# Kernel optimization log

Measured on AMD Instinct MI355X. Metric: run time of the kernel, lower is better.

Reference implementation:

```python
import jax, jax.numpy as jnp
import numpy as np

B, T, C, HS = 256, 256, 384, 64

def setup_inputs() -> dict:
    key = jax.random.key(0)
    ks = jax.random.split(key, 7)
    return {
        "x": jax.random.normal(ks[0], (B, T, C), dtype=jnp.float32),
        "Wq": jax.random.normal(ks[1], (C, HS), dtype=jnp.float32) * (C ** -0.5),
        "bq": jax.random.normal(ks[2], (HS,), dtype=jnp.float32) * 0.02,
        "Wk": jax.random.normal(ks[3], (C, HS), dtype=jnp.float32) * (C ** -0.5),
        "bk": jax.random.normal(ks[4], (HS,), dtype=jnp.float32) * 0.02,
        "Wv": jax.random.normal(ks[5], (C, HS), dtype=jnp.float32) * (C ** -0.5),
        "bv": jax.random.normal(ks[6], (HS,), dtype=jnp.float32) * 0.02,
    }

def reference(x, Wq, bq, Wk, bk, Wv, bv):
    # single-head causal self-attention (eval mode: dropout is identity)
    T_ = x.shape[1]
    q = x @ Wq + bq          # [B, T, HS]
    k = x @ Wk + bk          # [B, T, HS]
    v = x @ Wv + bv          # [B, T, HS]
    scale = k.shape[-1] ** -0.5
    att = jnp.einsum("btd,bsd->bts", q, k) * scale   # [B, T, T]
    causal = jnp.tril(jnp.ones((T_, T_), dtype=bool))  # tril buffer
    att = jnp.where(causal, att, -jnp.inf)             # mask future positions
    att = jax.nn.softmax(att, axis=-1)
    return jnp.einsum("bts,bsd->btd", att, v)          # [B, T, HS]
```

## Files before the change

kernel.cpp:

```cpp
#include <hip/hip_runtime.h>
#include <hip/hip_bf16.h>

#define BB 256
#define TT 256
#define CC 384
#define HSS 64

typedef __bf16 bf16_t;
typedef bf16_t bf16x8 __attribute__((ext_vector_type(8)));
typedef bf16_t bf16x4 __attribute__((ext_vector_type(4)));
typedef float f32x4 __attribute__((ext_vector_type(4)));

__device__ __forceinline__ f32x4 mfma16(bf16x8 a, bf16x8 b, f32x4 c) {
    return __builtin_amdgcn_mfma_f32_16x16x32_bf16(a, b, c, 0, 0, 0);
}

__device__ __forceinline__ bf16x8 cvt8(float4 a, float4 b) {
    bf16x8 r;
    r[0] = (bf16_t)a.x; r[1] = (bf16_t)a.y; r[2] = (bf16_t)a.z; r[3] = (bf16_t)a.w;
    r[4] = (bf16_t)b.x; r[5] = (bf16_t)b.y; r[6] = (bf16_t)b.z; r[7] = (bf16_t)b.w;
    return r;
}

typedef __attribute__((address_space(3))) unsigned int lds_uint_t;
typedef const __attribute__((address_space(1))) unsigned int glb_uint_t;
__device__ __forceinline__ void async_cp16(const void* g, void* lds_uniform) {
    __builtin_amdgcn_global_load_lds((glb_uint_t*)g, (lds_uint_t*)lds_uniform, 16, 0, 0);
}

__global__ void prep_w(const float* __restrict__ Wq, const float* __restrict__ Wk,
                       const float* __restrict__ Wv, bf16_t* __restrict__ WtG) {
    int idx = blockIdx.x * 256 + threadIdx.x;
    if (idx >= 192 * 384) return;
    int n = idx / 384, k = idx % 384;
    const float* W = (n < 64) ? Wq : (n < 128) ? Wk : Wv;
    float val = W[k * 64 + (n & 63)];
    int kc = k >> 6, kin = k & 63;
    int c = kin >> 3, e = k & 7;
    int pc = c ^ (n & 7);
    WtG[kc * 12288 + n * 64 + pc * 8 + e] = (bf16_t)val;
}

__global__ __attribute__((amdgpu_flat_work_group_size(512, 512),
                          amdgpu_waves_per_eu(2, 2)))
void head_fused(
    const float* __restrict__ x, const bf16_t* __restrict__ WtG,
    const float* __restrict__ bq, const float* __restrict__ bk, const float* __restrict__ bv,
    float* __restrict__ out) {

    __shared__ bf16_t Wl[2][12288];
    __shared__ uint4 Ksw[2048];
    __shared__ uint4 Vsw[2048];
    __shared__ __align__(16) bf16_t Pb[8 * 640];

    int b = blockIdx.x, tid = threadIdx.x;
    int w = tid >> 6, l = tid & 63, lr = l & 15, lq = l >> 4;
    int Mt[2] = {w, 15 - w};

    float bqv[4], bkv[4], bvv[4];
#pragma unroll
    for (int nt = 0; nt < 4; nt++) {
        bqv[nt] = bq[nt * 16 + lr];
        bkv[nt] = bk[nt * 16 + lr];
        bvv[nt] = bv[nt * 16 + lr];
    }

    const float* xr[2];
    xr[0] = x + ((size_t)b * TT + Mt[0] * 16 + lr) * CC;
    xr[1] = x + ((size_t)b * TT + Mt[1] * 16 + lr) * CC;

    f32x4 acc[2][12];
#pragma unroll
    for (int m = 0; m < 2; m++)
#pragma unroll
        for (int i = 0; i < 12; i++) acc[m][i] = (f32x4){0.f, 0.f, 0.f, 0.f};

    float4 xf[2][2][2];

#define DMA_CHUNK(kc, buf)                                                   \
    {                                                                        \
        const bf16_t* _src = WtG + (kc) * 12288;                             \
        _Pragma("unroll")                                                    \
        for (int j = 0; j < 3; j++) {                                        \
            int cbase = (j * 8 + w) * 64;   \
            async_cp16(_src + (size_t)(cbase + l) * 8,                       \
                       &Wl[buf][(size_t)cbase * 8]);                         \
        }                                                                    \
    }
#define LOAD_X(kc)                                                           \
    {                                                                        \
        _Pragma("unroll")                                                    \
        for (int m = 0; m < 2; m++)                                          \
            _Pragma("unroll")                                                \
            for (int t = 0; t < 2; t++) {                                    \
                const float* xp = xr[m] + (kc) * 64 + t * 32 + lq * 8;       \
                xf[m][t][0] = *(const float4*)xp;                            \
                xf[m][t][1] = *(const float4*)(xp + 4);                      \
            }                                                                \
    }

    DMA_CHUNK(0, 0);
    LOAD_X(0);

#pragma unroll
    for (int kc = 0; kc < 6; kc++) {
        __syncthreads();
        bf16x8 af[2][2];
#pragma unroll
        for (int m = 0; m < 2; m++)
#pragma unroll
            for (int t = 0; t < 2; t++) af[m][t] = cvt8(xf[m][t][0], xf[m][t][1]);
        if (kc < 5) {
            DMA_CHUNK(kc + 1, (kc + 1) & 1);
            LOAD_X(kc + 1);
        }
        const bf16_t* buf = Wl[kc & 1];
#pragma unroll
        for (int nt = 0; nt < 12; nt++) {
            const bf16_t* wl = buf + (size_t)(nt * 16 + lr) * 64;
#pragma unroll
            for (int t = 0; t < 2; t++) {
                int pc = (t * 4 + lq) ^ (lr & 7);
                bf16x8 bfrag = *(const bf16x8*)(wl + pc * 8);
                acc[0][nt] = mfma16(af[0][t], bfrag, acc[0][nt]);
                acc[1][nt] = mfma16(af[1][t], bfrag, acc[1][nt]);
            }
        }
    }
#undef DMA_CHUNK
#undef LOAD_X

    bf16_t* KswB = (bf16_t*)Ksw;
    bf16_t* VswB = (bf16_t*)Vsw;
#pragma unroll
    for (int m = 0; m < 2; m++) {
#pragma unroll
        for (int nt = 4; nt < 8; nt++) {
            int d = (nt - 4) * 16 + lr;
#pragma unroll
            for (int r = 0; r < 4; r++) {
                int s = Mt[m] * 16 + lq * 4 + r;
                KswB[s * 64 + ((d >> 3) ^ (s & 7)) * 8 + (d & 7)] =
                    (bf16_t)(acc[m][nt][r] + bkv[nt - 4]);
            }
        }
#pragma unroll
        for (int nt = 8; nt < 12; nt++) {
            int d = (nt - 8) * 16 + lr;
            int t0 = Mt[m] * 16 + lq * 4;
            int c = t0 >> 3;
            bf16x4 pk;
#pragma unroll
            for (int r = 0; r < 4; r++) pk[r] = (bf16_t)(acc[m][nt][r] + bvv[nt - 8]);
            *(bf16x4*)(VswB + d * 256 + ((c & ~7) | ((c ^ d) & 7)) * 8 + (t0 & 7)) = pk;
        }
    }
    __syncthreads();

    const float scale2 = 0.125f * 1.4426950408889634f;
    bf16_t* Pw = Pb + w * 640;

#pragma unroll
    for (int m = 0; m < 2; m++) {
        int R0 = Mt[m] * 16;
        int tg = R0 + lr;
        int ktm = Mt[m] >> 1;

        bf16x8 qf[2];
#pragma unroll
        for (int hh = 0; hh < 2; hh++) {
#pragma unroll
            for (int u = 0; u < 2; u++) {
                int nt = 2 * hh + u;
#pragma unroll
                for (int r = 0; r < 4; r++)
                    Pw[(lq * 4 + r) * 40 + u * 16 + lr] =
                        (bf16_t)(acc[m][nt][r] + bqv[nt]);
            }
            qf[hh] = *(const bf16x8*)(Pw + lr * 40 + lq * 8);
        }

        f32x4 oacc[4] = {};
        float sum = 0.f;
#pragma unroll
        for (int kt = 0; kt < 8; kt++) {
            if (kt <= ktm) {
#pragma unroll
                for (int u = 0; u < 2; u++) {
                    int nt = kt * 2 + u;
                    int s = nt * 16 + lr;
                    const uint4* krow = Ksw + s * 8;
                    bf16x8 k0 = __builtin_bit_cast(bf16x8, krow[lq ^ (s & 7)]);
                    bf16x8 k1 = __builtin_bit_cast(bf16x8, krow[(4 + lq) ^ (s & 7)]);
                    f32x4 a = {0.f, 0.f, 0.f, 0.f};
                    a = mfma16(k0, qf[0], a);
                    a = mfma16(k1, qf[1], a);
                    bf16x4 pk;
#pragma unroll
                    for (int r = 0; r < 4; r++) {
                        int sg = nt * 16 + lq * 4 + r;
                        float p = (sg <= tg) ? exp2f(a[r] * scale2) : 0.f;
                        sum += p;
                        pk[r] = (bf16_t)p;
                    }
                    *(bf16x4*)(Pw + lr * 40 + u * 16 + lq * 4) = pk;
                }
                bf16x8 pf = *(const bf16x8*)(Pw + lr * 40 + lq * 8);
#pragma unroll
                for (int dt = 0; dt < 4; dt++) {
                    int d = dt * 16 + lr;
                    int cc = kt * 4 + lq;
                    bf16x8 vf = __builtin_bit_cast(bf16x8,
                        Vsw[d * 32 + ((cc & ~7) | ((cc ^ d) & 7))]);
                    oacc[dt] = mfma16(vf, pf, oacc[dt]);
                }
            }
        }

        sum += __shfl_xor(sum, 16);
        sum += __shfl_xor(sum, 32);
        float inv = 1.0f / sum;

        float* orow = out + ((size_t)b * TT + R0 + lr) * HSS;
#pragma unroll
        for (int dt = 0; dt < 4; dt++) {
            float4 o;
            o.x = oacc[dt][0] * inv;
            o.y = oacc[dt][1] * inv;
            o.z = oacc[dt][2] * inv;
            o.w = oacc[dt][3] * inv;
            *(float4*)(orow + dt * 16 + lq * 4) = o;
        }
    }
}

extern "C" void kernel_launch(void* const* d_in, const int* in_sizes, int n_in,
                              void* d_out, int out_size, void* d_ws, size_t ws_size,
                              hipStream_t stream) {
    const float* x  = (const float*)d_in[0];
    const float* Wq = (const float*)d_in[1];
    const float* bq = (const float*)d_in[2];
    const float* Wk = (const float*)d_in[3];
    const float* bk = (const float*)d_in[4];
    const float* Wv = (const float*)d_in[5];
    const float* bv = (const float*)d_in[6];
    float* out = (float*)d_out;

    bf16_t* WtG = (bf16_t*)d_ws;

    prep_w<<<288, 256, 0, stream>>>(Wq, Wk, Wv, WtG);
    head_fused<<<BB, 512, 0, stream>>>(x, WtG, bq, bk, bv, out);
}
```

Measured before the change: 176.0 us.

## Use 16 waves per block with one query tile per wave

The block grows from 512 to 1024 threads, and each of 16 waves now owns a single 16-row tile instead of a paired front/back tile. Each wave does half the projection MFMAs and needs fewer accumulator registers, which is meant to raise waves per EU and hide latency. The cost is losing the causal load balancing the tile pairing gave: waves with late tiles do up to eight times the attention work of early ones, so the block finishes at the pace of the slowest wave. The weight DMA is split across 16 waves with a conditional second copy.

```diff
diff --git a/kernel.cpp b/kernel.cpp
--- a/kernel.cpp
+++ b/kernel.cpp
@@ -41,8 +41,8 @@
     WtG[kc * 12288 + n * 64 + pc * 8 + e] = (bf16_t)val;
 }
 
-__global__ __attribute__((amdgpu_flat_work_group_size(512, 512),
-                          amdgpu_waves_per_eu(2, 2)))
+__global__ __attribute__((amdgpu_flat_work_group_size(1024, 1024),
+                          amdgpu_waves_per_eu(4, 4)))
 void head_fused(
     const float* __restrict__ x, const bf16_t* __restrict__ WtG,
     const float* __restrict__ bq, const float* __restrict__ bk, const float* __restrict__ bv,
@@ -51,11 +51,11 @@
     __shared__ bf16_t Wl[2][12288];
     __shared__ uint4 Ksw[2048];
     __shared__ uint4 Vsw[2048];
-    __shared__ __align__(16) bf16_t Pb[8 * 640];
+    __shared__ __align__(16) bf16_t Pb[16 * 640];
 
     int b = blockIdx.x, tid = threadIdx.x;
     int w = tid >> 6, l = tid & 63, lr = l & 15, lq = l >> 4;
-    int Mt[2] = {w, 15 - w};
+    int Mt = w;
 
     float bqv[4], bkv[4], bvv[4];
 #pragma unroll
@@ -65,38 +65,34 @@
         bvv[nt] = bv[nt * 16 + lr];
     }
 
-    const float* xr[2];
-    xr[0] = x + ((size_t)b * TT + Mt[0] * 16 + lr) * CC;
-    xr[1] = x + ((size_t)b * TT + Mt[1] * 16 + lr) * CC;
-
-    f32x4 acc[2][12];
-#pragma unroll
-    for (int m = 0; m < 2; m++)
-#pragma unroll
-        for (int i = 0; i < 12; i++) acc[m][i] = (f32x4){0.f, 0.f, 0.f, 0.f};
-
-    float4 xf[2][2][2];
+    const float* xr = x + ((size_t)b * TT + Mt * 16 + lr) * CC;
+
+    f32x4 acc[12];
+#pragma unroll
+    for (int i = 0; i < 12; i++) acc[i] = (f32x4){0.f, 0.f, 0.f, 0.f};
+
+    float4 xf[2][2];
 
 #define DMA_CHUNK(kc, buf)                                                   \
     {                                                                        \
         const bf16_t* _src = WtG + (kc) * 12288;                             \
-        _Pragma("unroll")                                                    \
-        for (int j = 0; j < 3; j++) {                                        \
-            int cbase = (j * 8 + w) * 64;   \
-            async_cp16(_src + (size_t)(cbase + l) * 8,                       \
-                       &Wl[buf][(size_t)cbase * 8]);                         \
+        int cb0 = w * 64;                                                    \
+        async_cp16(_src + (size_t)(cb0 + l) * 8,                             \
+                   &Wl[buf][(size_t)cb0 * 8]);                               \
+        if (w < 8) {                                                         \
+            int cb1 = (16 + w) * 64;                                         \
+            async_cp16(_src + (size_t)(cb1 + l) * 8,                         \
+                       &Wl[buf][(size_t)cb1 * 8]);                           \
         }                                                                    \
     }
 #define LOAD_X(kc)                                                           \
     {                                                                        \
         _Pragma("unroll")                                                    \
-        for (int m = 0; m < 2; m++)                                          \
-            _Pragma("unroll")                                                \
-            for (int t = 0; t < 2; t++) {                                    \
-                const float* xp = xr[m] + (kc) * 64 + t * 32 + lq * 8;       \
-                xf[m][t][0] = *(const float4*)xp;                            \
-                xf[m][t][1] = *(const float4*)(xp + 4);                      \
-            }                                                                \
+        for (int t = 0; t < 2; t++) {                                        \
+            const float* xp = xr + (kc) * 64 + t * 32 + lq * 8;              \
+            xf[t][0] = *(const float4*)xp;                                   \
+            xf[t][1] = *(const float4*)(xp + 4);                             \
+        }                                                                    \
     }
 
     DMA_CHUNK(0, 0);
@@ -105,11 +101,9 @@
 #pragma unroll
     for (int kc = 0; kc < 6; kc++) {
         __syncthreads();
-        bf16x8 af[2][2];
-#pragma unroll
-        for (int m = 0; m < 2; m++)
-#pragma unroll
-            for (int t = 0; t < 2; t++) af[m][t] = cvt8(xf[m][t][0], xf[m][t][1]);
+        bf16x8 af[2];
+#pragma unroll
+        for (int t = 0; t < 2; t++) af[t] = cvt8(xf[t][0], xf[t][1]);
         if (kc < 5) {
             DMA_CHUNK(kc + 1, (kc + 1) & 1);
             LOAD_X(kc + 1);
@@ -122,8 +116,7 @@
             for (int t = 0; t < 2; t++) {
                 int pc = (t * 4 + lq) ^ (lr & 7);
                 bf16x8 bfrag = *(const bf16x8*)(wl + pc * 8);
-                acc[0][nt] = mfma16(af[0][t], bfrag, acc[0][nt]);
-                acc[1][nt] = mfma16(af[1][t], bfrag, acc[1][nt]);
+                acc[nt] = mfma16(af[t], bfrag, acc[nt]);
             }
         }
     }
@@ -133,104 +126,98 @@
     bf16_t* KswB = (bf16_t*)Ksw;
     bf16_t* VswB = (bf16_t*)Vsw;
 #pragma unroll
-    for (int m = 0; m < 2; m++) {
-#pragma unroll
-        for (int nt = 4; nt < 8; nt++) {
-            int d = (nt - 4) * 16 + lr;
-#pragma unroll
-            for (int r = 0; r < 4; r++) {
-                int s = Mt[m] * 16 + lq * 4 + r;
-                KswB[s * 64 + ((d >> 3) ^ (s & 7)) * 8 + (d & 7)] =
-                    (bf16_t)(acc[m][nt][r] + bkv[nt - 4]);
-            }
-        }
-#pragma unroll
-        for (int nt = 8; nt < 12; nt++) {
-            int d = (nt - 8) * 16 + lr;
-            int t0 = Mt[m] * 16 + lq * 4;
-            int c = t0 >> 3;
-            bf16x4 pk;
-#pragma unroll
-            for (int r = 0; r < 4; r++) pk[r] = (bf16_t)(acc[m][nt][r] + bvv[nt - 8]);
-            *(bf16x4*)(VswB + d * 256 + ((c & ~7) | ((c ^ d) & 7)) * 8 + (t0 & 7)) = pk;
-        }
+    for (int nt = 4; nt < 8; nt++) {
+        int d = (nt - 4) * 16 + lr;
+#pragma unroll
+        for (int r = 0; r < 4; r++) {
+            int s = Mt * 16 + lq * 4 + r;
+            KswB[s * 64 + ((d >> 3) ^ (s & 7)) * 8 + (d & 7)] =
+                (bf16_t)(acc[nt][r] + bkv[nt - 4]);
+        }
+    }
+#pragma unroll
+    for (int nt = 8; nt < 12; nt++) {
+        int d = (nt - 8) * 16 + lr;
+        int t0 = Mt * 16 + lq * 4;
+        int c = t0 >> 3;
+        bf16x4 pk;
+#pragma unroll
+        for (int r = 0; r < 4; r++) pk[r] = (bf16_t)(acc[nt][r] + bvv[nt - 8]);
+        *(bf16x4*)(VswB + d * 256 + ((c & ~7) | ((c ^ d) & 7)) * 8 + (t0 & 7)) = pk;
     }
     __syncthreads();
 
     const float scale2 = 0.125f * 1.4426950408889634f;
     bf16_t* Pw = Pb + w * 640;
 
-#pragma unroll
-    for (int m = 0; m < 2; m++) {
-        int R0 = Mt[m] * 16;
-        int tg = R0 + lr;
-        int ktm = Mt[m] >> 1;
-
-        bf16x8 qf[2];
-#pragma unroll
-        for (int hh = 0; hh < 2; hh++) {
+    int R0 = Mt * 16;
+    int tg = R0 + lr;
+    int ktm = Mt >> 1;
+
+    bf16x8 qf[2];
+#pragma unroll
+    for (int hh = 0; hh < 2; hh++) {
+#pragma unroll
+        for (int u = 0; u < 2; u++) {
+            int nt = 2 * hh + u;
+#pragma unroll
+            for (int r = 0; r < 4; r++)
+                Pw[(lq * 4 + r) * 40 + u * 16 + lr] =
+                    (bf16_t)(acc[nt][r] + bqv[nt]);
+        }
+        qf[hh] = *(const bf16x8*)(Pw + lr * 40 + lq * 8);
+    }
+
+    f32x4 oacc[4] = {};
+    float sum = 0.f;
+#pragma unroll
+    for (int kt = 0; kt < 8; kt++) {
+        if (kt <= ktm) {
 #pragma unroll
             for (int u = 0; u < 2; u++) {
-                int nt = 2 * hh + u;
-#pragma unroll
-                for (int r = 0; r < 4; r++)
-                    Pw[(lq * 4 + r) * 40 + u * 16 + lr] =
-                        (bf16_t)(acc[m][nt][r] + bqv[nt]);
+                int nt = kt * 2 + u;
+                int s = nt * 16 + lr;
+                const uint4* krow = Ksw + s * 8;
+                bf16x8 k0 = __builtin_bit_cast(bf16x8, krow[lq ^ (s & 7)]);
+                bf16x8 k1 = __builtin_bit_cast(bf16x8, krow[(4 + lq) ^ (s & 7)]);
+                f32x4 a = {0.f, 0.f, 0.f, 0.f};
+                a = mfma16(k0, qf[0], a);
+                a = mfma16(k1, qf[1], a);
+                bf16x4 pk;
+#pragma unroll
+                for (int r = 0; r < 4; r++) {
+                    int sg = nt * 16 + lq * 4 + r;
+                    float p = (sg <= tg) ? exp2f(a[r] * scale2) : 0.f;
+                    sum += p;
+                    pk[r] = (bf16_t)p;
+                }
+                *(bf16x4*)(Pw + lr * 40 + u * 16 + lq * 4) = pk;
             }
-            qf[hh] = *(const bf16x8*)(Pw + lr * 40 + lq * 8);
-        }
-
-        f32x4 oacc[4] = {};
-        float sum = 0.f;
-#pragma unroll
-        for (int kt = 0; kt < 8; kt++) {
-            if (kt <= ktm) {
-#pragma unroll
-                for (int u = 0; u < 2; u++) {
-                    int nt = kt * 2 + u;
-                    int s = nt * 16 + lr;
-                    const uint4* krow = Ksw + s * 8;
-                    bf16x8 k0 = __builtin_bit_cast(bf16x8, krow[lq ^ (s & 7)]);
-                    bf16x8 k1 = __builtin_bit_cast(bf16x8, krow[(4 + lq) ^ (s & 7)]);
-                    f32x4 a = {0.f, 0.f, 0.f, 0.f};
-                    a = mfma16(k0, qf[0], a);
-                    a = mfma16(k1, qf[1], a);
-                    bf16x4 pk;
-#pragma unroll
-                    for (int r = 0; r < 4; r++) {
-                        int sg = nt * 16 + lq * 4 + r;
-                        float p = (sg <= tg) ? exp2f(a[r] * scale2) : 0.f;
-                        sum += p;
-                        pk[r] = (bf16_t)p;
-                    }
-                    *(bf16x4*)(Pw + lr * 40 + u * 16 + lq * 4) = pk;
-                }
-                bf16x8 pf = *(const bf16x8*)(Pw + lr * 40 + lq * 8);
-#pragma unroll
-                for (int dt = 0; dt < 4; dt++) {
-                    int d = dt * 16 + lr;
-                    int cc = kt * 4 + lq;
-                    bf16x8 vf = __builtin_bit_cast(bf16x8,
-                        Vsw[d * 32 + ((cc & ~7) | ((cc ^ d) & 7))]);
-                    oacc[dt] = mfma16(vf, pf, oacc[dt]);
-                }
+            bf16x8 pf = *(const bf16x8*)(Pw + lr * 40 + lq * 8);
+#pragma unroll
+            for (int dt = 0; dt < 4; dt++) {
+                int d = dt * 16 + lr;
+                int cc = kt * 4 + lq;
+                bf16x8 vf = __builtin_bit_cast(bf16x8,
+                    Vsw[d * 32 + ((cc & ~7) | ((cc ^ d) & 7))]);
+                oacc[dt] = mfma16(vf, pf, oacc[dt]);
             }
         }
-
-        sum += __shfl_xor(sum, 16);
-        sum += __shfl_xor(sum, 32);
-        float inv = 1.0f / sum;
-
-        float* orow = out + ((size_t)b * TT + R0 + lr) * HSS;
-#pragma unroll
-        for (int dt = 0; dt < 4; dt++) {
-            float4 o;
-            o.x = oacc[dt][0] * inv;
-            o.y = oacc[dt][1] * inv;
-            o.z = oacc[dt][2] * inv;
-            o.w = oacc[dt][3] * inv;
-            *(float4*)(orow + dt * 16 + lq * 4) = o;
-        }
+    }
+
+    sum += __shfl_xor(sum, 16);
+    sum += __shfl_xor(sum, 32);
+    float inv = 1.0f / sum;
+
+    float* orow = out + ((size_t)b * TT + R0 + lr) * HSS;
+#pragma unroll
+    for (int dt = 0; dt < 4; dt++) {
+        float4 o;
+        o.x = oacc[dt][0] * inv;
+        o.y = oacc[dt][1] * inv;
+        o.z = oacc[dt][2] * inv;
+        o.w = oacc[dt][3] * inv;
+        *(float4*)(orow + dt * 16 + lq * 4) = o;
     }
 }
 
@@ -249,5 +236,5 @@
     bf16_t* WtG = (bf16_t*)d_ws;
 
     prep_w<<<288, 256, 0, stream>>>(Wq, Wk, Wv, WtG);
-    head_fused<<<BB, 512, 0, stream>>>(x, WtG, bq, bk, bv, out);
-}
+    head_fused<<<BB, 1024, 0, stream>>>(x, WtG, bq, bk, bv, out);
+}
```

Result: no change. 173.8 us (-1.2%).
